# Kernel tuning notes

Hardware: AMD Instinct MI355X
Metric: run time of the kernel (lower is better)

The kernel has to match this reference:

```python
import jax, jax.numpy as jnp
import numpy as np

B, N, K, F_IN, F_OUT = 2, 196608, 9, 64, 64


def setup_inputs() -> dict:
    key = jax.random.key(0)
    k1, k2, k3 = jax.random.split(key, 3)
    x = jax.random.normal(k1, (B, N, F_IN), dtype=jnp.float32)
    adjc = jax.random.randint(k2, (N, K), 0, N, dtype=jnp.int64)
    # first neighbor is the cell itself (typical grid adjacency)
    adjc = adjc.at[:, 0].set(jnp.arange(N, dtype=jnp.int64))
    scale = 1.0 / np.sqrt(K * F_IN)
    W = jax.random.normal(k3, (K, F_IN, F_OUT), dtype=jnp.float32) * scale
    b = jnp.zeros((F_OUT,), dtype=jnp.float32)
    return {"x": x, "adjc": adjc, "W": W, "b": b}


def reference(x, adjc, W, b):
    # get_nh: irregular gather of neighbor features -> [B, N, K, F_in]
    x_nh = x[:, adjc, :]
    # learned layer: contract over (neighborhood, in_features) -> [B, N, F_out]
    out = jnp.einsum("bnkf,kfo->bno", x_nh, W) + b
    return out
```

## Files before the change

### kernel.cpp

```cpp
#include <hip/hip_runtime.h>

#define B_ 2
#define N_ 196608
#define K_ 9
#define F_ 64
#define ROWS 64
#define ROWB 256

typedef __attribute__((ext_vector_type(8))) short short8;
typedef __attribute__((ext_vector_type(4))) unsigned short ushort4v;
typedef __attribute__((ext_vector_type(4))) float f32x4;

__device__ __forceinline__ unsigned short f2bf(float f) {
  unsigned u = __builtin_bit_cast(unsigned, f);
  u = (u + 0x7fffu + ((u >> 16) & 1u)) >> 16;
  return (unsigned short)u;
}

__global__ __launch_bounds__(256) void cvt_x_kernel(const float* __restrict__ x,
                                                    unsigned short* __restrict__ xb) {
  const int b = blockIdx.y;
  const long cidx = (long)blockIdx.x * 256 + threadIdx.x;
  const long n = cidx >> 4;
  const int qd = (int)(cidx & 15);
  const float4 v = *(const float4*)(x + ((size_t)b * N_ + n) * F_ + (size_t)qd * 4);
  ushort4v r;
  r[0] = f2bf(v.x); r[1] = f2bf(v.y); r[2] = f2bf(v.z); r[3] = f2bf(v.w);
  *(ushort4v*)(xb + ((size_t)n * 2 + b) * F_ + qd * 4) = r;
}

__global__ __launch_bounds__(256) void cvt_w_kernel(const float* __restrict__ W,
                                                    unsigned short* __restrict__ wt) {
  const int i = blockIdx.x * 256 + threadIdx.x;
  const int k = i >> 12;
  const int rem = i & 4095;
  const int o = rem >> 6;
  const int f = rem & 63;
  wt[i] = f2bf(W[(k << 12) + (f << 6) + o]);
}

__global__ __launch_bounds__(256, 3) void nhconv_main(
    const short* __restrict__ xb,
    const int* __restrict__ adjc,
    const short* __restrict__ wt,
    const float* __restrict__ bias,
    float* __restrict__ out) {
  __shared__ short abuf[3][ROWS * 128];
  __shared__ int s_adj[ROWS * K_];

  const int tid = (int)threadIdx.x;
  const int n0 = blockIdx.x * ROWS;
  const int w = tid >> 6;
  const int l = tid & 63;
  const int q = l >> 4;
  const int c = l & 15;

  {
    const int base = w * (16 * K_);
    for (int i = l; i < 16 * K_; i += 64)
      s_adj[base + i] =
          __builtin_nontemporal_load(adjc + (size_t)(n0 + w * 16) * K_ + i);
  }

  auto stage = [&](int k, int bf) {
#pragma unroll
    for (int j = 0; j < 4; ++j) {
      const int row = w * 16 + j * 4 + (l >> 4);
      const int src_chunk = (l & 15) ^ (row & 7);
      const size_t goff = (size_t)(unsigned)s_adj[row * K_ + k] * ROWB + (src_chunk << 4);
      const char* src = (const char*)xb + goff;
      short* dst = &abuf[bf][(w * 16 + j * 4) * 128];
      __builtin_amdgcn_global_load_lds(
          (const __attribute__((address_space(1))) unsigned int*)src,
          (__attribute__((address_space(3))) unsigned int*)dst, 16, 0, 0);
    }
  };

  const short* wbase = wt + q * 8 + (c << 6);
  short8 rw[2][8];
  auto wload = [&](int k, int par) {
#pragma unroll
    for (int fs = 0; fs < 2; ++fs)
#pragma unroll
      for (int ct = 0; ct < 4; ++ct)
        rw[par][fs * 4 + ct] = *(const short8*)(wbase + (k << 12) + fs * 32 + (ct << 10));
  };

  f32x4 acc[2][4];
#pragma unroll
  for (int p = 0; p < 2; ++p)
#pragma unroll
    for (int ct = 0; ct < 4; ++ct)
      acc[p][ct] = (f32x4){0.f, 0.f, 0.f, 0.f};

  wload(0, 0);
  stage(0, 0);
  wload(1, 1);
  stage(1, 1);

#pragma unroll
  for (int k = 0; k < K_; ++k) {
    asm volatile("s_waitcnt lgkmcnt(0)" ::: "memory");
    if (k >= 1 && k + 1 < K_) wload(k + 1, (k + 1) & 1);
    if (k + 2 < K_) stage(k + 2, (k + 2) % 3);

    if (k <= K_ - 3) {
      asm volatile("s_waitcnt vmcnt(16)" ::: "memory");
    } else if (k == K_ - 2) {
      asm volatile("s_waitcnt vmcnt(12)" ::: "memory");
    } else {
      asm volatile("s_waitcnt vmcnt(0)" ::: "memory");
    }
    __builtin_amdgcn_sched_barrier(0);

    const short* bufk = abuf[k % 3];
    const int arow = (w * 16 + c) * 128;
#pragma unroll
    for (int fs = 0; fs < 2; ++fs) {
      const int ch0 = (fs * 4 + q) ^ (c & 7);
      const int ch1 = (8 + fs * 4 + q) ^ (c & 7);
      const short8 a0 = *(const short8*)&bufk[arow + (ch0 << 3)];
      const short8 a1 = *(const short8*)&bufk[arow + (ch1 << 3)];
#pragma unroll
      for (int ct = 0; ct < 4; ++ct) {
        const short8 bfr = rw[k & 1][fs * 4 + ct];
        acc[0][ct] = __builtin_amdgcn_mfma_f32_16x16x32_bf16(a0, bfr, acc[0][ct], 0, 0, 0);
        acc[1][ct] = __builtin_amdgcn_mfma_f32_16x16x32_bf16(a1, bfr, acc[1][ct], 0, 0, 0);
      }
    }
  }

  float bv[4];
#pragma unroll
  for (int ct = 0; ct < 4; ++ct) bv[ct] = bias[ct * 16 + c];

#pragma unroll
  for (int p = 0; p < 2; ++p) {
    const size_t outbase = ((size_t)p * N_ + (size_t)(n0 + w * 16)) * F_;
#pragma unroll
    for (int ct = 0; ct < 4; ++ct) {
#pragma unroll
      for (int rr = 0; rr < 4; ++rr) {
        const int row = q * 4 + rr;
        __builtin_nontemporal_store(acc[p][ct][rr] + bv[ct],
                                    &out[outbase + (size_t)row * F_ + ct * 16 + c]);
      }
    }
  }
}

extern "C" void kernel_launch(void* const* d_in, const int* in_sizes, int n_in,
                              void* d_out, int out_size, void* d_ws, size_t ws_size,
                              hipStream_t stream) {
  const float* x = (const float*)d_in[0];
  const int* adjc = (const int*)d_in[1];
  const float* W = (const float*)d_in[2];
  const float* bias = (const float*)d_in[3];
  float* out = (float*)d_out;

  unsigned short* xb = (unsigned short*)d_ws;
  unsigned short* wt = (unsigned short*)((char*)d_ws + (size_t)B_ * N_ * F_ * 2);

  cvt_x_kernel<<<dim3(N_ * 16 / 256, B_), 256, 0, stream>>>(x, xb);
  cvt_w_kernel<<<144, 256, 0, stream>>>(W, wt);

  nhconv_main<<<N_ / ROWS, 256, 0, stream>>>((const short*)xb, adjc, (const short*)wt,
                                             bias, out);
}
```

Baseline: 297.4 us.

## Process all 64 rows per single-wave block to reuse weight registers

The block shrinks from four waves of 16 rows each to one wave that covers all 64 rows with four row tiles. Each weight fragment loaded into registers now feeds four times as many MFMAs, which cuts repeated weight loads from global memory. The wave issues 16 gathers per neighbor stage, and the vmcnt thresholds are raised to match. The cost is far fewer resident waves per CU: LDS use per block is unchanged while each block now holds only one wave. That weakens latency hiding for the irregular gather, and the 128-float accumulator raises register pressure.

```diff
diff --git a/kernel.cpp b/kernel.cpp
--- a/kernel.cpp
+++ b/kernel.cpp
@@ -39,7 +39,7 @@
   wt[i] = f2bf(W[(k << 12) + (f << 6) + o]);
 }
 
-__global__ __launch_bounds__(256, 3) void nhconv_main(
+__global__ __launch_bounds__(64, 1) void nhconv_main(
     const short* __restrict__ xb,
     const int* __restrict__ adjc,
     const short* __restrict__ wt,
@@ -48,28 +48,22 @@
   __shared__ short abuf[3][ROWS * 128];
   __shared__ int s_adj[ROWS * K_];
 
-  const int tid = (int)threadIdx.x;
+  const int l = (int)threadIdx.x;
   const int n0 = blockIdx.x * ROWS;
-  const int w = tid >> 6;
-  const int l = tid & 63;
   const int q = l >> 4;
   const int c = l & 15;
 
-  {
-    const int base = w * (16 * K_);
-    for (int i = l; i < 16 * K_; i += 64)
-      s_adj[base + i] =
-          __builtin_nontemporal_load(adjc + (size_t)(n0 + w * 16) * K_ + i);
-  }
+  for (int i = l; i < ROWS * K_; i += 64)
+    s_adj[i] = __builtin_nontemporal_load(adjc + (size_t)n0 * K_ + i);
 
   auto stage = [&](int k, int bf) {
 #pragma unroll
-    for (int j = 0; j < 4; ++j) {
-      const int row = w * 16 + j * 4 + (l >> 4);
+    for (int j = 0; j < 16; ++j) {
+      const int row = j * 4 + (l >> 4);
       const int src_chunk = (l & 15) ^ (row & 7);
       const size_t goff = (size_t)(unsigned)s_adj[row * K_ + k] * ROWB + (src_chunk << 4);
       const char* src = (const char*)xb + goff;
-      short* dst = &abuf[bf][(w * 16 + j * 4) * 128];
+      short* dst = &abuf[bf][(j * 4) * 128];
       __builtin_amdgcn_global_load_lds(
           (const __attribute__((address_space(1))) unsigned int*)src,
           (__attribute__((address_space(3))) unsigned int*)dst, 16, 0, 0);
@@ -86,12 +80,14 @@
         rw[par][fs * 4 + ct] = *(const short8*)(wbase + (k << 12) + fs * 32 + (ct << 10));
   };
 
-  f32x4 acc[2][4];
+  f32x4 acc[2][4][4];
 #pragma unroll
   for (int p = 0; p < 2; ++p)
 #pragma unroll
-    for (int ct = 0; ct < 4; ++ct)
-      acc[p][ct] = (f32x4){0.f, 0.f, 0.f, 0.f};
+    for (int rt = 0; rt < 4; ++rt)
+#pragma unroll
+      for (int ct = 0; ct < 4; ++ct)
+        acc[p][rt][ct] = (f32x4){0.f, 0.f, 0.f, 0.f};
 
   wload(0, 0);
   stage(0, 0);
@@ -105,27 +101,32 @@
     if (k + 2 < K_) stage(k + 2, (k + 2) % 3);
 
     if (k <= K_ - 3) {
-      asm volatile("s_waitcnt vmcnt(16)" ::: "memory");
+      asm volatile("s_waitcnt vmcnt(40)" ::: "memory");
     } else if (k == K_ - 2) {
-      asm volatile("s_waitcnt vmcnt(12)" ::: "memory");
+      asm volatile("s_waitcnt vmcnt(24)" ::: "memory");
     } else {
       asm volatile("s_waitcnt vmcnt(0)" ::: "memory");
     }
     __builtin_amdgcn_sched_barrier(0);
 
     const short* bufk = abuf[k % 3];
-    const int arow = (w * 16 + c) * 128;
 #pragma unroll
     for (int fs = 0; fs < 2; ++fs) {
-      const int ch0 = (fs * 4 + q) ^ (c & 7);
-      const int ch1 = (8 + fs * 4 + q) ^ (c & 7);
-      const short8 a0 = *(const short8*)&bufk[arow + (ch0 << 3)];
-      const short8 a1 = *(const short8*)&bufk[arow + (ch1 << 3)];
 #pragma unroll
-      for (int ct = 0; ct < 4; ++ct) {
-        const short8 bfr = rw[k & 1][fs * 4 + ct];
-        acc[0][ct] = __builtin_amdgcn_mfma_f32_16x16x32_bf16(a0, bfr, acc[0][ct], 0, 0, 0);
-        acc[1][ct] = __builtin_amdgcn_mfma_f32_16x16x32_bf16(a1, bfr, acc[1][ct], 0, 0, 0);
+      for (int rt = 0; rt < 4; ++rt) {
+        const int arow = (rt * 16 + c) * 128;
+        const int ch0 = (fs * 4 + q) ^ (c & 7);
+        const int ch1 = (8 + fs * 4 + q) ^ (c & 7);
+        const short8 a0 = *(const short8*)&bufk[arow + (ch0 << 3)];
+        const short8 a1 = *(const short8*)&bufk[arow + (ch1 << 3)];
+#pragma unroll
+        for (int ct = 0; ct < 4; ++ct) {
+          const short8 bfr = rw[k & 1][fs * 4 + ct];
+          acc[0][rt][ct] =
+              __builtin_amdgcn_mfma_f32_16x16x32_bf16(a0, bfr, acc[0][rt][ct], 0, 0, 0);
+          acc[1][rt][ct] =
+              __builtin_amdgcn_mfma_f32_16x16x32_bf16(a1, bfr, acc[1][rt][ct], 0, 0, 0);
+        }
       }
     }
   }
@@ -136,14 +137,17 @@
 
 #pragma unroll
   for (int p = 0; p < 2; ++p) {
-    const size_t outbase = ((size_t)p * N_ + (size_t)(n0 + w * 16)) * F_;
+    const size_t outbase = ((size_t)p * N_ + (size_t)n0) * F_;
 #pragma unroll
-    for (int ct = 0; ct < 4; ++ct) {
+    for (int rt = 0; rt < 4; ++rt) {
 #pragma unroll
-      for (int rr = 0; rr < 4; ++rr) {
-        const int row = q * 4 + rr;
-        __builtin_nontemporal_store(acc[p][ct][rr] + bv[ct],
-                                    &out[outbase + (size_t)row * F_ + ct * 16 + c]);
+      for (int ct = 0; ct < 4; ++ct) {
+#pragma unroll
+        for (int rr = 0; rr < 4; ++rr) {
+          const int row = rt * 16 + q * 4 + rr;
+          __builtin_nontemporal_store(acc[p][rt][ct][rr] + bv[ct],
+                                      &out[outbase + (size_t)row * F_ + ct * 16 + c]);
+        }
       }
     }
   }
@@ -164,6 +168,6 @@
   cvt_x_kernel<<<dim3(N_ * 16 / 256, B_), 256, 0, stream>>>(x, xb);
   cvt_w_kernel<<<144, 256, 0, stream>>>(W, wt);
 
-  nhconv_main<<<N_ / ROWS, 256, 0, stream>>>((const short*)xb, adjc, (const short*)wt,
-                                             bias, out);
+  nhconv_main<<<N_ / ROWS, 64, 0, stream>>>((const short*)xb, adjc, (const short*)wt,
+                                            bias, out);
 }
```

Result: faster. 263.5 us (-11.4%).
